# Optimization experiments

Hardware: AMD Instinct MI355X
Metric: run time of the kernel (lower is better)

## Reference

```python
import jax, jax.numpy as jnp
import numpy as np

DIM = 192
K = 3
RED = 4
B, H, W = 4, 256, 256
EPS = 1e-5  # BatchNorm eps

def _make_mask():
    # PixelCNN mask type 'A': zero the center pixel and everything after it
    m = np.ones((DIM, 1, K, K), np.float32)
    m[:, :, K // 2, K // 2:] = 0.0  # center row: center col onward
    m[:, :, K // 2 + 1:] = 0.0      # all rows below center
    return jnp.asarray(m)

MASK = _make_mask()  # [DIM, 1, K, K]

def setup_inputs() -> dict:
    key = jax.random.key(0)
    ks = jax.random.split(key, 4)
    r = DIM // RED
    return {
        "x": jax.random.normal(ks[0], (B, DIM, H, W), jnp.float32),
        "w1": jax.random.normal(ks[1], (r, DIM), jnp.float32) * 0.05,      # conv1 1x1, no bias
        "gamma": jnp.ones((r,), jnp.float32),                               # BN weight
        "beta": jnp.zeros((r,), jnp.float32),                               # BN bias
        "running_mean": jnp.zeros((r,), jnp.float32),
        "running_var": jnp.ones((r,), jnp.float32),
        "w2": jax.random.normal(ks[2], (DIM * K * K, r), jnp.float32) * 0.05,  # conv2 1x1
        "b2": jnp.zeros((DIM * K * K,), jnp.float32),
        "bias": jnp.zeros((DIM,), jnp.float32),                             # depthwise conv bias
    }

def reference(x, w1, gamma, beta, running_mean, running_var, w2, b2, bias):
    b, c, h, w = x.shape  # c == DIM
    # --- dynamic weight generation: pool -> 1x1 conv -> BN(eval) -> ReLU -> 1x1 conv ---
    pooled = x.mean(axis=(2, 3))                                   # [b, dim]
    t = pooled @ w1.T                                              # [b, dim//red]
    t = gamma * (t - running_mean) * jax.lax.rsqrt(running_var + EPS) + beta
    t = jax.nn.relu(t)
    wt = t @ w2.T + b2                                             # [b, dim*K*K]
    wt = wt.reshape(b * DIM, 1, K, K) * jnp.tile(MASK, (b, 1, 1, 1))
    # --- per-sample masked depthwise conv via batch-folding (groups = b*dim) ---
    out = jax.lax.conv_general_dilated(
        x.reshape(1, b * c, h, w), wt,
        window_strides=(1, 1), padding=((1, 1), (1, 1)),
        feature_group_count=b * DIM,
        dimension_numbers=("NCHW", "OIHW", "NCHW"))                # [1, b*dim, h, w]
    out = out + jnp.tile(bias, (b,))[None, :, None, None]
    return out.reshape(b, c, h, w)
```

## Files before the change

### kernel.cpp

```cpp
#include <hip/hip_runtime.h>

#define DIMC 192
#define HID  48
#define HW   65536
#define WIDTH 256
#define NPLANE 768

__global__ __launch_bounds__(1024) void k_pool(const float* __restrict__ x,
                                               float* __restrict__ pooled) {
    const int plane = blockIdx.x;
    const float4* p = (const float4*)(x + (size_t)plane * HW);
    const int t = threadIdx.x;
    float s = 0.f;
#pragma unroll
    for (int k = 0; k < 16; ++k) {
        float4 v = p[k * 1024 + t];
        s += (v.x + v.y) + (v.z + v.w);
    }
#pragma unroll
    for (int off = 32; off > 0; off >>= 1) s += __shfl_down(s, off, 64);
    __shared__ float wsum[16];
    const int wave = t >> 6, lane = t & 63;
    if (lane == 0) wsum[wave] = s;
    __syncthreads();
    if (t == 0) {
        float tot = 0.f;
#pragma unroll
        for (int i = 0; i < 16; ++i) tot += wsum[i];
        pooled[plane] = tot * (1.0f / 65536.0f);
    }
}

__global__ __launch_bounds__(256) void k_weights(
    const float* __restrict__ pooled,
    const float* __restrict__ w1,
    const float* __restrict__ gamma,
    const float* __restrict__ beta,
    const float* __restrict__ rmean,
    const float* __restrict__ rvar,
    const float* __restrict__ w2,
    const float* __restrict__ b2,
    float* __restrict__ w4)
{
    const int b = blockIdx.x;
    const int tid = threadIdx.x;
    __shared__ float P[DIMC];
    __shared__ float T[HID];
    if (tid < DIMC) P[tid] = pooled[b * DIMC + tid];
    __syncthreads();
    if (tid < HID) {
        const float* wr = w1 + tid * DIMC;
        float acc = 0.f;
        for (int d = 0; d < DIMC; ++d) acc += P[d] * wr[d];
        const float inv = 1.0f / sqrtf(rvar[tid] + 1e-5f);
        float v = gamma[tid] * (acc - rmean[tid]) * inv + beta[tid];
        T[tid] = v > 0.f ? v : 0.f;
    }
    __syncthreads();
    for (int idx = tid; idx < DIMC * 4; idx += 256) {
        const int c = idx >> 2, tap = idx & 3;
        const int o = c * 9 + tap;
        const float* wr = w2 + o * HID;
        float acc = b2[o];
        for (int j = 0; j < HID; ++j) acc += T[j] * wr[j];
        w4[b * DIMC * 4 + idx] = acc;
    }
}

__global__ __launch_bounds__(256) void k_conv(const float* __restrict__ x,
                                              const float4* __restrict__ w4,
                                              const float* __restrict__ bias,
                                              float* __restrict__ out) {
    const int plane = blockIdx.x >> 3;
    const int c = plane % DIMC;
    const int wave = threadIdx.x >> 6;
    const int lane = threadIdx.x & 63;
    const int y0 = ((blockIdx.x & 7) << 5) + (wave << 3);
    const float4 wt = w4[plane];
    const float bs = bias[c];
    const float4* xp = (const float4*)(x + (size_t)plane * HW);
    float4* op = (float4*)(out + (size_t)plane * HW);

    float4 a;
    if (y0 == 0) a = make_float4(0.f, 0.f, 0.f, 0.f);
    else         a = xp[(y0 - 1) * 64 + lane];

#pragma unroll
    for (int r = 0; r < 8; ++r) {
        const int y = y0 + r;
        float4 bb = xp[y * 64 + lane];
        float leftA  = __shfl_up(a.w, 1, 64);   if (lane == 0)  leftA  = 0.f;
        float rightA = __shfl_down(a.x, 1, 64); if (lane == 63) rightA = 0.f;
        float leftB  = __shfl_up(bb.w, 1, 64);  if (lane == 0)  leftB  = 0.f;
        float4 o;
        o.x = wt.x * leftA + wt.y * a.x + wt.z * a.y   + wt.w * leftB + bs;
        o.y = wt.x * a.x   + wt.y * a.y + wt.z * a.z   + wt.w * bb.x  + bs;
        o.z = wt.x * a.y   + wt.y * a.z + wt.z * a.w   + wt.w * bb.y  + bs;
        o.w = wt.x * a.z   + wt.y * a.w + wt.z * rightA + wt.w * bb.z + bs;
        op[y * 64 + lane] = o;
        a = bb;
    }
}

extern "C" void kernel_launch(void* const* d_in, const int* in_sizes, int n_in,
                              void* d_out, int out_size, void* d_ws, size_t ws_size,
                              hipStream_t stream) {
    const float* x     = (const float*)d_in[0];
    const float* w1    = (const float*)d_in[1];
    const float* gamma = (const float*)d_in[2];
    const float* beta  = (const float*)d_in[3];
    const float* rmean = (const float*)d_in[4];
    const float* rvar  = (const float*)d_in[5];
    const float* w2    = (const float*)d_in[6];
    const float* b2    = (const float*)d_in[7];
    const float* bias  = (const float*)d_in[8];
    float* out = (float*)d_out;

    float* pooled = (float*)d_ws;
    float* w4     = pooled + NPLANE;

    k_pool<<<NPLANE, 1024, 0, stream>>>(x, pooled);
    k_weights<<<4, 256, 0, stream>>>(pooled, w1, gamma, beta, rmean, rvar, w2, b2, w4);
    k_conv<<<NPLANE * 8, 256, 0, stream>>>(x, (const float4*)w4, bias, out);
}
```

Baseline: 394.0 us.

## Fuse pool, weight generation and masked conv into one cooperative kernel

Replaces the three kernel launches with one cooperative kernel of 256 blocks of 1024 threads. Each block pools three planes, a grid sync precedes weight generation in four blocks, and a second grid sync precedes each block convolving its same three planes. The aim is to remove launch gaps and to catch the re-read of x in L2 or MALL, since each block reads planes it just pooled. In exchange, 256 blocks on 256 CUs gives low occupancy and latency hiding, the weight phase runs serially inside the grid, and two grid-wide barriers are added.

```diff
diff --git a/kernel.cpp b/kernel.cpp
--- a/kernel.cpp
+++ b/kernel.cpp
@@ -1,38 +1,17 @@
 #include <hip/hip_runtime.h>
+#include <hip/hip_cooperative_groups.h>
+
+namespace cg = cooperative_groups;
 
 #define DIMC 192
 #define HID  48
 #define HW   65536
-#define WIDTH 256
 #define NPLANE 768
+#define NBLK 256
+#define PPB 3
 
-__global__ __launch_bounds__(1024) void k_pool(const float* __restrict__ x,
-                                               float* __restrict__ pooled) {
-    const int plane = blockIdx.x;
-    const float4* p = (const float4*)(x + (size_t)plane * HW);
-    const int t = threadIdx.x;
-    float s = 0.f;
-#pragma unroll
-    for (int k = 0; k < 16; ++k) {
-        float4 v = p[k * 1024 + t];
-        s += (v.x + v.y) + (v.z + v.w);
-    }
-#pragma unroll
-    for (int off = 32; off > 0; off >>= 1) s += __shfl_down(s, off, 64);
-    __shared__ float wsum[16];
-    const int wave = t >> 6, lane = t & 63;
-    if (lane == 0) wsum[wave] = s;
-    __syncthreads();
-    if (t == 0) {
-        float tot = 0.f;
-#pragma unroll
-        for (int i = 0; i < 16; ++i) tot += wsum[i];
-        pooled[plane] = tot * (1.0f / 65536.0f);
-    }
-}
-
-__global__ __launch_bounds__(256) void k_weights(
-    const float* __restrict__ pooled,
+__global__ __launch_bounds__(1024) void fused_kernel(
+    const float* __restrict__ x,
     const float* __restrict__ w1,
     const float* __restrict__ gamma,
     const float* __restrict__ beta,
@@ -40,65 +19,94 @@
     const float* __restrict__ rvar,
     const float* __restrict__ w2,
     const float* __restrict__ b2,
-    float* __restrict__ w4)
+    const float* __restrict__ bias,
+    float* __restrict__ out,
+    float* __restrict__ pooled,
+    float* __restrict__ w4v)
 {
-    const int b = blockIdx.x;
-    const int tid = threadIdx.x;
-    __shared__ float P[DIMC];
+    cg::grid_group grid = cg::this_grid();
+    const int blk  = blockIdx.x;
+    const int t    = threadIdx.x;
+    const int wave = t >> 6;
+    const int lane = t & 63;
+
+    __shared__ float wsum[16];
     __shared__ float T[HID];
-    if (tid < DIMC) P[tid] = pooled[b * DIMC + tid];
-    __syncthreads();
-    if (tid < HID) {
-        const float* wr = w1 + tid * DIMC;
-        float acc = 0.f;
-        for (int d = 0; d < DIMC; ++d) acc += P[d] * wr[d];
-        const float inv = 1.0f / sqrtf(rvar[tid] + 1e-5f);
-        float v = gamma[tid] * (acc - rmean[tid]) * inv + beta[tid];
-        T[tid] = v > 0.f ? v : 0.f;
+
+    for (int pi = 0; pi < PPB; ++pi) {
+        const int plane = blk * PPB + pi;
+        const float4* p = (const float4*)(x + (size_t)plane * HW);
+        float s = 0.f;
+#pragma unroll
+        for (int k = 0; k < 16; ++k) {
+            float4 v = p[k * 1024 + t];
+            s += (v.x + v.y) + (v.z + v.w);
+        }
+#pragma unroll
+        for (int off = 32; off > 0; off >>= 1) s += __shfl_down(s, off, 64);
+        if (lane == 0) wsum[wave] = s;
+        __syncthreads();
+        if (t == 0) {
+            float tot = 0.f;
+#pragma unroll
+            for (int i = 0; i < 16; ++i) tot += wsum[i];
+            pooled[plane] = tot * (1.0f / 65536.0f);
+        }
+        __syncthreads();
     }
-    __syncthreads();
-    for (int idx = tid; idx < DIMC * 4; idx += 256) {
-        const int c = idx >> 2, tap = idx & 3;
-        const int o = c * 9 + tap;
-        const float* wr = w2 + o * HID;
-        float acc = b2[o];
-        for (int j = 0; j < HID; ++j) acc += T[j] * wr[j];
-        w4[b * DIMC * 4 + idx] = acc;
+    grid.sync();
+
+    if (blk < 4) {
+        if (t < HID) {
+            const float* wr = w1 + t * DIMC;
+            const float* P  = pooled + blk * DIMC;
+            float acc = 0.f;
+            for (int d = 0; d < DIMC; ++d) acc += P[d] * wr[d];
+            const float inv = 1.0f / sqrtf(rvar[t] + 1e-5f);
+            float v = gamma[t] * (acc - rmean[t]) * inv + beta[t];
+            T[t] = v > 0.f ? v : 0.f;
+        }
+        __syncthreads();
+        if (t < DIMC * 4) {
+            const int c = t >> 2, tap = t & 3;
+            const int o = c * 9 + tap;
+            const float* wr = w2 + o * HID;
+            float acc = b2[o];
+            for (int j = 0; j < HID; ++j) acc += T[j] * wr[j];
+            w4v[blk * DIMC * 4 + t] = acc;
+        }
     }
-}
+    grid.sync();
 
-__global__ __launch_bounds__(256) void k_conv(const float* __restrict__ x,
-                                              const float4* __restrict__ w4,
-                                              const float* __restrict__ bias,
-                                              float* __restrict__ out) {
-    const int plane = blockIdx.x >> 3;
-    const int c = plane % DIMC;
-    const int wave = threadIdx.x >> 6;
-    const int lane = threadIdx.x & 63;
-    const int y0 = ((blockIdx.x & 7) << 5) + (wave << 3);
-    const float4 wt = w4[plane];
-    const float bs = bias[c];
-    const float4* xp = (const float4*)(x + (size_t)plane * HW);
-    float4* op = (float4*)(out + (size_t)plane * HW);
+    const float4* w4p = (const float4*)w4v;
+    for (int pi = 0; pi < PPB; ++pi) {
+        const int plane = blk * PPB + pi;
+        const int c = plane % DIMC;
+        const float4 wt = w4p[plane];
+        const float bs = bias[c];
+        const float4* xp = (const float4*)(x + (size_t)plane * HW);
+        float4* op = (float4*)(out + (size_t)plane * HW);
 
-    float4 a;
-    if (y0 == 0) a = make_float4(0.f, 0.f, 0.f, 0.f);
-    else         a = xp[(y0 - 1) * 64 + lane];
+        const int y0 = wave << 4;
+        float4 a;
+        if (y0 == 0) a = make_float4(0.f, 0.f, 0.f, 0.f);
+        else         a = xp[(y0 - 1) * 64 + lane];
 
 #pragma unroll
-    for (int r = 0; r < 8; ++r) {
-        const int y = y0 + r;
-        float4 bb = xp[y * 64 + lane];
-        float leftA  = __shfl_up(a.w, 1, 64);   if (lane == 0)  leftA  = 0.f;
-        float rightA = __shfl_down(a.x, 1, 64); if (lane == 63) rightA = 0.f;
-        float leftB  = __shfl_up(bb.w, 1, 64);  if (lane == 0)  leftB  = 0.f;
-        float4 o;
-        o.x = wt.x * leftA + wt.y * a.x + wt.z * a.y   + wt.w * leftB + bs;
-        o.y = wt.x * a.x   + wt.y * a.y + wt.z * a.z   + wt.w * bb.x  + bs;
-        o.z = wt.x * a.y   + wt.y * a.z + wt.z * a.w   + wt.w * bb.y  + bs;
-        o.w = wt.x * a.z   + wt.y * a.w + wt.z * rightA + wt.w * bb.z + bs;
-        op[y * 64 + lane] = o;
-        a = bb;
+        for (int r = 0; r < 16; ++r) {
+            const int y = y0 + r;
+            float4 bb = xp[y * 64 + lane];
+            float leftA  = __shfl_up(a.w, 1, 64);   if (lane == 0)  leftA  = 0.f;
+            float rightA = __shfl_down(a.x, 1, 64); if (lane == 63) rightA = 0.f;
+            float leftB  = __shfl_up(bb.w, 1, 64);  if (lane == 0)  leftB  = 0.f;
+            float4 o;
+            o.x = wt.x * leftA + wt.y * a.x + wt.z * a.y    + wt.w * leftB + bs;
+            o.y = wt.x * a.x   + wt.y * a.y + wt.z * a.z    + wt.w * bb.x  + bs;
+            o.z = wt.x * a.y   + wt.y * a.z + wt.z * a.w    + wt.w * bb.y  + bs;
+            o.w = wt.x * a.z   + wt.y * a.w + wt.z * rightA + wt.w * bb.z  + bs;
+            op[y * 64 + lane] = o;
+            a = bb;
+        }
     }
 }
 
@@ -119,7 +127,11 @@
     float* pooled = (float*)d_ws;
     float* w4     = pooled + NPLANE;
 
-    k_pool<<<NPLANE, 1024, 0, stream>>>(x, pooled);
-    k_weights<<<4, 256, 0, stream>>>(pooled, w1, gamma, beta, rmean, rvar, w2, b2, w4);
-    k_conv<<<NPLANE * 8, 256, 0, stream>>>(x, (const float4*)w4, bias, out);
+    void* args[] = {
+        (void*)&x, (void*)&w1, (void*)&gamma, (void*)&beta, (void*)&rmean,
+        (void*)&rvar, (void*)&w2, (void*)&b2, (void*)&bias, (void*)&out,
+        (void*)&pooled, (void*)&w4,
+    };
+    hipLaunchCooperativeKernel((void*)fused_kernel, dim3(NBLK), dim3(1024),
+                               args, 0, stream);
 }
```

Result: slower. 464.9 us (+18.0%).
